# Kernel tuning notes

Hardware: AMD Instinct MI355X
Metric: run time of the kernel (lower is better)

The kernel has to match this reference:

```python
import jax, jax.numpy as jnp
import numpy as np

N_NODES = 50000
N_EDGES = 500000
H = 128
N_LAYERS = 3


def _mlp_params(key, in_dim, h_dim, out_dim):
    k1, k2 = jax.random.split(key)
    s1 = 1.0 / np.sqrt(in_dim)
    s2 = 1.0 / np.sqrt(h_dim)
    return (jax.random.uniform(k1, (in_dim, h_dim), jnp.float32, -s1, s1),
            jnp.zeros((h_dim,), jnp.float32),
            jax.random.uniform(k2, (h_dim, out_dim), jnp.float32, -s2, s2),
            jnp.zeros((out_dim,), jnp.float32))


def setup_inputs() -> dict:
    key = jax.random.key(0)
    ks = jax.random.split(key, 8)
    x = jax.random.normal(ks[0], (N_NODES, H), jnp.float32)
    edge_attr = jax.random.normal(ks[1], (N_EDGES, H), jnp.float32)
    pos = jax.random.normal(ks[2], (N_NODES, 3), jnp.float32)
    src = jax.random.randint(ks[3], (N_EDGES,), 0, N_NODES)
    # avoid self-loops so rel_dist > 0 (original assumes no zero-length edges)
    off = jax.random.randint(ks[4], (N_EDGES,), 1, N_NODES)
    dst = (src + off) % N_NODES
    edge_index = jnp.stack([src, dst]).astype(jnp.int64)
    # per-layer MLP params, stacked over layers
    msg, acc, nod = [], [], []
    for i in range(N_LAYERS):
        kk = jax.random.fold_in(ks[5], i)
        ka, kb, kc = jax.random.split(kk, 3)
        msg.append(_mlp_params(ka, 3 * H, H, H))       # message_mlp
        acc.append(_mlp_params(kb, H, 2 * H, 1))       # accl_mlp
        nod.append(_mlp_params(kc, 2 * H, 2 * H, H))   # node_mlp
    stack = lambda ps: tuple(jnp.stack([p[j] for p in ps]) for j in range(4))
    mW1, mb1, mW2, mb2 = stack(msg)
    aW1, ab1, aW2, ab2 = stack(acc)
    nW1, nb1, nW2, nb2 = stack(nod)
    return dict(x=x, edge_index=edge_index, edge_attr=edge_attr, pos=pos,
                msg_W1=mW1, msg_b1=mb1, msg_W2=mW2, msg_b2=mb2,
                acc_W1=aW1, acc_b1=ab1, acc_W2=aW2, acc_b2=ab2,
                node_W1=nW1, node_b1=nb1, node_W2=nW2, node_b2=nb2)


def _mlp(h, W1, b1, W2, b2):
    return jax.nn.relu(h @ W1 + b1) @ W2 + b2


def reference(x, edge_index, edge_attr, pos,
              msg_W1, msg_b1, msg_W2, msg_b2,
              acc_W1, acc_b1, acc_W2, acc_b2,
              node_W1, node_b1, node_W2, node_b2):
    src, dst = edge_index[0], edge_index[1]
    n = x.shape[0]
    deg = jax.ops.segment_sum(jnp.ones((src.shape[0],), x.dtype), dst, num_segments=n)
    denom = jnp.maximum(deg, 1.0)[:, None]
    for l in range(N_LAYERS):
        # message: cat(x_i=dst, x_j=src, edge_attr) -> MLP
        m_in = jnp.concatenate([x[dst], x[src], edge_attr], axis=-1)  # [E, 3H]
        m = _mlp(m_in, msg_W1[l], msg_b1[l], msg_W2[l], msg_b2[l])    # [E, H]
        # equivariant acceleration update
        w = _mlp(m, acc_W1[l], acc_b1[l], acc_W2[l], acc_b2[l])       # [E, 1]
        rel = pos[src] - pos[dst]                                     # [E, 3]
        dist = jnp.sqrt(jnp.sum(rel * rel, axis=-1, keepdims=True))
        acc_e = w * rel / dist
        pos = pos + jax.ops.segment_sum(acc_e, dst, num_segments=n) / denom
        # node update (beta_x = 1.0 -> x_out = x_update)
        intra = jax.ops.segment_sum(m, dst, num_segments=n) / denom   # [N, H]
        x = _mlp(jnp.concatenate([x, intra], axis=-1),
                 node_W1[l], node_b1[l], node_W2[l], node_b2[l])
    return pos
```

## Files before the change

### kernel.cpp

```cpp
#include <hip/hip_runtime.h>
#include <hip/hip_bf16.h>
#include <math.h>

#define N_NODES 50000
#define N_EDGES 500000
#define H 128
#define NL 3
#define SCAN_B 256
#define NCHUNK ((N_NODES + SCAN_B - 1) / SCAN_B)

typedef short short8v __attribute__((ext_vector_type(8)));
typedef float f32x4 __attribute__((ext_vector_type(4)));
typedef unsigned short ushort8v __attribute__((ext_vector_type(8)));
typedef unsigned short ushort4v __attribute__((ext_vector_type(4)));

__device__ __forceinline__ unsigned short f2b(float f) {
  __hip_bfloat16 h = __float2bfloat16(f);
  return __builtin_bit_cast(unsigned short, h);
}
__device__ __forceinline__ float b2f(unsigned short s) {
  unsigned u = (unsigned)s << 16;
  return __builtin_bit_cast(float, u);
}


__global__ void k_deg_i(const int* __restrict__ dst, int* __restrict__ degC) {
  int e = blockIdx.x * blockDim.x + threadIdx.x;
  if (e < N_EDGES) atomicAdd(&degC[dst[e]], 1);
}

__global__ void k_inv(const int* __restrict__ degC, float* __restrict__ invd) {
  int i = blockIdx.x * blockDim.x + threadIdx.x;
  if (i < N_NODES) invd[i] = 1.0f / fmaxf((float)degC[i], 1.0f);
}

__global__ void k_scan1(const int* __restrict__ degC, int* __restrict__ cursor,
                        int* __restrict__ chunkSum) {
  __shared__ int s[SCAN_B];
  int t = threadIdx.x, i = blockIdx.x * SCAN_B + t;
  int v = (i < N_NODES) ? degC[i] : 0;
  s[t] = v;
  __syncthreads();
  for (int o = 1; o < SCAN_B; o <<= 1) {
    int u = (t >= o) ? s[t - o] : 0;
    __syncthreads();
    s[t] += u;
    __syncthreads();
  }
  if (i < N_NODES) cursor[i] = s[t] - v;
  if (t == SCAN_B - 1) chunkSum[blockIdx.x] = s[t];
}

__global__ void k_scan2(int* __restrict__ chunkSum) {
  __shared__ int s[SCAN_B];
  int t = threadIdx.x;
  int v = (t < NCHUNK) ? chunkSum[t] : 0;
  s[t] = v;
  __syncthreads();
  for (int o = 1; o < SCAN_B; o <<= 1) {
    int u = (t >= o) ? s[t - o] : 0;
    __syncthreads();
    s[t] += u;
    __syncthreads();
  }
  if (t < NCHUNK) chunkSum[t] = s[t] - v;
}

__global__ void k_scan3(int* __restrict__ cursor, const int* __restrict__ chunkSum) {
  int i = blockIdx.x * SCAN_B + threadIdx.x;
  if (i < N_NODES) cursor[i] += chunkSum[blockIdx.x];
}

__global__ void k_scatter_sort(const int* __restrict__ dst, int* __restrict__ cursor,
                               int* __restrict__ sorted) {
  int e = blockIdx.x * blockDim.x + threadIdx.x;
  if (e < N_EDGES) {
    int p = atomicAdd(&cursor[dst[e]], 1);
    sorted[p] = e;
  }
}


__global__ void k_cvt_x(const float* __restrict__ x, unsigned short* __restrict__ xb, int n4) {
  int i = blockIdx.x * blockDim.x + threadIdx.x;
  if (i < n4) {
    float4 v = ((const float4*)x)[i];
    ushort4v o;
    o[0] = f2b(v.x); o[1] = f2b(v.y); o[2] = f2b(v.z); o[3] = f2b(v.w);
    ((ushort4v*)xb)[i] = o;
  }
}

__global__ void k_cvt_wt(const float* __restrict__ src, unsigned short* __restrict__ dst,
                         int K, int N, int total) {
  int i = blockIdx.x * blockDim.x + threadIdx.x;
  if (i < total) {
    int l = i / (K * N);
    int rem = i - l * K * N;
    int k = rem / N;
    int n = rem - k * N;
    dst[((size_t)l * N + n) * K + k] = f2b(src[i]);
  }
}

#define MFMA_STEP(AP, APITCH, AKOFF, ACCN)                                         \
  { _Pragma("unroll")                                                              \
    for (int ks = 0; ks < 2; ++ks) {                                               \
      short8v af_ = *(const short8v*)&AP[(wv * 16 + ln15) * APITCH + (AKOFF) + ks * 32 + quad * 8]; \
      _Pragma("unroll")                                                            \
      for (int nt = 0; nt < 8; ++nt) {                                             \
        short8v bf_ = *(const short8v*)&sB[(nt * 16 + ln15) * 72 + ks * 32 + quad * 8]; \
        ACCN[nt] = __builtin_amdgcn_mfma_f32_16x16x32_bf16(af_, bf_, ACCN[nt], 0, 0, 0); \
      } } }

#define STAGE_B(EXPR)                                                              \
  { _Pragma("unroll")                                                              \
    for (int i_ = 0; i_ < 4; ++i_) {                                               \
      int flat_ = tid + i_ * 256;                                                  \
      int n = flat_ >> 3, seg = flat_ & 7;                                         \
      *(float4*)&sB[n * 72 + seg * 8] = *(const float4*)&(EXPR);                   \
    } }


__launch_bounds__(256, 4)
__global__ void k_xab(const unsigned short* __restrict__ xb,
                      const unsigned short* __restrict__ mW1t,
                      unsigned short* __restrict__ xab)
{
  __shared__ unsigned short sB[128 * 72];
  const int tid = threadIdx.x;
  const int n0 = blockIdx.x * 64;
  const int wv = tid >> 6, lane = tid & 63, quad = lane >> 4, ln15 = lane & 15;
  const int arow = min(n0 + wv * 16 + ln15, N_NODES - 1);

  short8v afr[2][2];
#pragma unroll
  for (int c = 0; c < 2; ++c)
#pragma unroll
    for (int ks = 0; ks < 2; ++ks)
      afr[c][ks] = *(const short8v*)&xb[(size_t)arow * H + c * 64 + ks * 32 + quad * 8];

  for (int h = 0; h < 2; ++h) {
    f32x4 acc[8];
#pragma unroll
    for (int nt = 0; nt < 8; ++nt) acc[nt] = (f32x4){0.f, 0.f, 0.f, 0.f};
    for (int c = 0; c < 2; ++c) {
      STAGE_B(mW1t[(size_t)n * 384 + h * 128 + c * 64 + seg * 8])
      __syncthreads();
#pragma unroll
      for (int ks = 0; ks < 2; ++ks) {
#pragma unroll
        for (int nt = 0; nt < 8; ++nt) {
          short8v bf = *(const short8v*)&sB[(nt * 16 + ln15) * 72 + ks * 32 + quad * 8];
          acc[nt] = __builtin_amdgcn_mfma_f32_16x16x32_bf16(afr[c][ks], bf, acc[nt], 0, 0, 0);
        }
      }
      __syncthreads();
    }
#pragma unroll
    for (int nt = 0; nt < 8; ++nt) {
      int col = nt * 16 + ln15;
#pragma unroll
      for (int r = 0; r < 4; ++r) {
        int row = n0 + wv * 16 + quad * 4 + r;
        if (row < N_NODES)
          xab[(size_t)row * 256 + h * 128 + col] = f2b(acc[nt][r]);
      }
    }
  }
}


__launch_bounds__(256, 4)
__global__ void k_edge(const unsigned short* __restrict__ xab,
                       const float* __restrict__ pos,
                       const float* __restrict__ eattr,
                       const int* __restrict__ srcI,
                       const int* __restrict__ dstI,
                       const int* __restrict__ sorted,
                       const unsigned short* __restrict__ mW1t, const float* __restrict__ mb1,
                       const unsigned short* __restrict__ mW2t, const float* __restrict__ mb2,
                       const unsigned short* __restrict__ aW1t, const float* __restrict__ ab1,
                       const float* __restrict__ aW2, const float* __restrict__ ab2,
                       float* __restrict__ intra,
                       float* __restrict__ pdelta,
                       int do_intra)
{
  __shared__ unsigned short sB[128 * 72];
  __shared__ unsigned short sM[64 * 136];
  __shared__ int sEid[64], sSrc[64], sDst[64];
  __shared__ float sW[64];
  __shared__ float sPE[64 * 3];

  const int tid = threadIdx.x;
  const int e0 = blockIdx.x * 64;
  const int nv = min(N_EDGES - e0, 64);
  if (tid < 64) {
    int idx = min(e0 + tid, N_EDGES - 1);
    int eid = sorted[idx];
    sEid[tid] = eid; sSrc[tid] = srcI[eid]; sDst[tid] = dstI[eid];
  }
  __syncthreads();

  const int wv = tid >> 6, lane = tid & 63, quad = lane >> 4, ln15 = lane & 15;

#pragma unroll
  for (int i_ = 0; i_ < 4; ++i_) {
    int flat = tid + i_ * 256;
    int row = flat >> 4, sg = flat & 15;
    ushort8v a = *(const ushort8v*)&xab[(size_t)sDst[row] * 256 + sg * 8];
    ushort8v b = *(const ushort8v*)&xab[(size_t)sSrc[row] * 256 + 128 + sg * 8];
    ushort8v o;
#pragma unroll
    for (int j = 0; j < 8; ++j) o[j] = f2b(b2f(a[j]) + b2f(b[j]));
    *(ushort8v*)&sM[row * 136 + sg * 8] = o;
  }

  f32x4 acc[8];
#pragma unroll
  for (int nt = 0; nt < 8; ++nt) acc[nt] = (f32x4){0.f, 0.f, 0.f, 0.f};

  const float* aep = eattr + (size_t)sEid[wv * 16 + ln15] * H;
  for (int c = 0; c < 2; ++c) {
    float4 q0 = *(const float4*)(aep + c * 64 + quad * 8);
    float4 q1 = *(const float4*)(aep + c * 64 + quad * 8 + 4);
    float4 q2 = *(const float4*)(aep + c * 64 + 32 + quad * 8);
    float4 q3 = *(const float4*)(aep + c * 64 + 32 + quad * 8 + 4);
    STAGE_B(mW1t[(size_t)n * 384 + 256 + c * 64 + seg * 8])
    __syncthreads();
    short8v af0, af1;
    af0[0] = (short)f2b(q0.x); af0[1] = (short)f2b(q0.y);
    af0[2] = (short)f2b(q0.z); af0[3] = (short)f2b(q0.w);
    af0[4] = (short)f2b(q1.x); af0[5] = (short)f2b(q1.y);
    af0[6] = (short)f2b(q1.z); af0[7] = (short)f2b(q1.w);
    af1[0] = (short)f2b(q2.x); af1[1] = (short)f2b(q2.y);
    af1[2] = (short)f2b(q2.z); af1[3] = (short)f2b(q2.w);
    af1[4] = (short)f2b(q3.x); af1[5] = (short)f2b(q3.y);
    af1[6] = (short)f2b(q3.z); af1[7] = (short)f2b(q3.w);
#pragma unroll
    for (int nt = 0; nt < 8; ++nt) {
      short8v bf = *(const short8v*)&sB[(nt * 16 + ln15) * 72 + quad * 8];
      acc[nt] = __builtin_amdgcn_mfma_f32_16x16x32_bf16(af0, bf, acc[nt], 0, 0, 0);
    }
#pragma unroll
    for (int nt = 0; nt < 8; ++nt) {
      short8v bf = *(const short8v*)&sB[(nt * 16 + ln15) * 72 + 32 + quad * 8];
      acc[nt] = __builtin_amdgcn_mfma_f32_16x16x32_bf16(af1, bf, acc[nt], 0, 0, 0);
    }
    __syncthreads();
  }

#pragma unroll
  for (int nt = 0; nt < 8; ++nt) {
    int col = nt * 16 + ln15;
    float bb = mb1[col];
#pragma unroll
    for (int r = 0; r < 4; ++r) {
      int row = wv * 16 + quad * 4 + r;
      float xv = b2f(sM[row * 136 + col]);
      sM[row * 136 + col] = f2b(fmaxf(acc[nt][r] + xv + bb, 0.f));
      acc[nt][r] = 0.f;
    }
  }
  __syncthreads();

  for (int c = 0; c < 2; ++c) {
    STAGE_B(mW2t[(size_t)n * 128 + c * 64 + seg * 8])
    __syncthreads();
    MFMA_STEP(sM, 136, c * 64, acc)
    __syncthreads();
  }

#pragma unroll
  for (int nt = 0; nt < 8; ++nt) {
    int col = nt * 16 + ln15;
    float bb = mb2[col];
#pragma unroll
    for (int r = 0; r < 4; ++r) {
      int row = wv * 16 + quad * 4 + r;
      sM[row * 136 + col] = f2b(acc[nt][r] + bb);
    }
  }
  __syncthreads();

  float wp0 = 0.f, wp1 = 0.f, wp2 = 0.f, wp3 = 0.f;
  for (int h = 0; h < 2; ++h) {
#pragma unroll
    for (int nt = 0; nt < 8; ++nt) acc[nt] = (f32x4){0.f, 0.f, 0.f, 0.f};
    for (int c = 0; c < 2; ++c) {
      STAGE_B(aW1t[((size_t)h * 128 + n) * 128 + c * 64 + seg * 8])
      __syncthreads();
      MFMA_STEP(sM, 136, c * 64, acc)
      __syncthreads();
    }
#pragma unroll
    for (int nt = 0; nt < 8; ++nt) {
      int col = h * 128 + nt * 16 + ln15;
      float bb = ab1[col], a2 = aW2[col];
      wp0 += fmaxf(acc[nt][0] + bb, 0.f) * a2;
      wp1 += fmaxf(acc[nt][1] + bb, 0.f) * a2;
      wp2 += fmaxf(acc[nt][2] + bb, 0.f) * a2;
      wp3 += fmaxf(acc[nt][3] + bb, 0.f) * a2;
    }
  }
#pragma unroll
  for (int m = 1; m <= 8; m <<= 1) {
    wp0 += __shfl_xor(wp0, m, 64);
    wp1 += __shfl_xor(wp1, m, 64);
    wp2 += __shfl_xor(wp2, m, 64);
    wp3 += __shfl_xor(wp3, m, 64);
  }
  if (ln15 == 0) {
    float b2 = ab2[0];
    sW[wv * 16 + quad * 4 + 0] = wp0 + b2;
    sW[wv * 16 + quad * 4 + 1] = wp1 + b2;
    sW[wv * 16 + quad * 4 + 2] = wp2 + b2;
    sW[wv * 16 + quad * 4 + 3] = wp3 + b2;
  }
  __syncthreads();

  if (tid < nv) {
    int s = sSrc[tid], d = sDst[tid];
    float rx = pos[s * 3 + 0] - pos[d * 3 + 0];
    float ry = pos[s * 3 + 1] - pos[d * 3 + 1];
    float rz = pos[s * 3 + 2] - pos[d * 3 + 2];
    float dist = sqrtf(rx * rx + ry * ry + rz * rz);
    float cf = sW[tid] / dist;
    sPE[tid * 3 + 0] = cf * rx;
    sPE[tid * 3 + 1] = cf * ry;
    sPE[tid * 3 + 2] = cf * rz;
  }
  __syncthreads();

  if (tid < 3) {
    float run = 0.0f;
    int cur = -2;
    for (int e = 0; e < 64; ++e) {
      int d = (e < nv) ? sDst[e] : -1;
      if (d != cur) {
        if (cur >= 0 && run != 0.0f) atomicAdd(&pdelta[cur * 3 + tid], run);
        run = 0.0f;
        cur = d;
      }
      if (d >= 0) run += sPE[e * 3 + tid];
    }
    if (cur >= 0 && run != 0.0f) atomicAdd(&pdelta[cur * 3 + tid], run);
  }

  if (do_intra) {
    int f = tid & 127;
    int hf = tid >> 7;
    int eBeg = hf * 32, eEnd = eBeg + 32;
    float run = 0.0f;
    int cur = -2;
    for (int e = eBeg; e < eEnd; ++e) {
      int d = (e < nv) ? sDst[e] : -1;
      if (d != cur) {
        if (cur >= 0 && run != 0.0f) atomicAdd(&intra[(size_t)cur * H + f], run);
        run = 0.0f;
        cur = d;
      }
      if (d >= 0) run += b2f(sM[e * 136 + f]);
    }
    if (cur >= 0 && run != 0.0f) atomicAdd(&intra[(size_t)cur * H + f], run);
  }
}


__launch_bounds__(256, 3)
__global__ void k_node(const unsigned short* __restrict__ xb,
                       const float* __restrict__ intra,
                       const float* __restrict__ invd,
                       const unsigned short* __restrict__ nW1t, const float* __restrict__ nb1,
                       const unsigned short* __restrict__ nW2t, const float* __restrict__ nb2,
                       const float* __restrict__ pos_in,
                       const float* __restrict__ pdelta,
                       unsigned short* __restrict__ xb_out,
                       float* __restrict__ pos_out,
                       int compute_x)
{
  __shared__ unsigned short sA[64 * 72];
  __shared__ unsigned short sB[128 * 72];
  __shared__ unsigned short sH[64 * 136];
  const int tid = threadIdx.x;
  const int n0 = blockIdx.x * 64;

  if (tid < 192) {
    int n = n0 + tid / 3, cc = tid % 3;
    if (n < N_NODES)
      pos_out[n * 3 + cc] = pos_in[n * 3 + cc] + pdelta[n * 3 + cc] * invd[n];
  }
  if (!compute_x) return;

  const int wv = tid >> 6, lane = tid & 63, quad = lane >> 4, ln15 = lane & 15;

  f32x4 xacc[8];
#pragma unroll
  for (int nt = 0; nt < 8; ++nt) xacc[nt] = (f32x4){0.f, 0.f, 0.f, 0.f};

  f32x4 acc[8];
  for (int h = 0; h < 2; ++h) {
#pragma unroll
    for (int nt = 0; nt < 8; ++nt) acc[nt] = (f32x4){0.f, 0.f, 0.f, 0.f};
    for (int c = 0; c < 4; ++c) {
#pragma unroll
      for (int i_ = 0; i_ < 2; ++i_) {
        int flat_ = tid + i_ * 256;
        int row = flat_ >> 3, seg = flat_ & 7;
        int n = min(n0 + row, N_NODES - 1);
        if (c < 2) {
          *(float4*)&sA[row * 72 + seg * 8] =
              *(const float4*)&xb[(size_t)n * H + c * 64 + seg * 8];
        } else {
          const float* ip = intra + (size_t)n * H + (c - 2) * 64 + seg * 8;
          float iv = invd[n];
          float4 p0 = *(const float4*)ip;
          float4 p1 = *(const float4*)(ip + 4);
          ushort8v v;
          v[0] = f2b(p0.x * iv); v[1] = f2b(p0.y * iv);
          v[2] = f2b(p0.z * iv); v[3] = f2b(p0.w * iv);
          v[4] = f2b(p1.x * iv); v[5] = f2b(p1.y * iv);
          v[6] = f2b(p1.z * iv); v[7] = f2b(p1.w * iv);
          *(ushort8v*)&sA[row * 72 + seg * 8] = v;
        }
      }
      STAGE_B(nW1t[((size_t)h * 128 + n) * 256 + c * 64 + seg * 8])
      __syncthreads();
      MFMA_STEP(sA, 72, 0, acc)
      __syncthreads();
    }
#pragma unroll
    for (int nt = 0; nt < 8; ++nt) {
      int col = nt * 16 + ln15;
      float bb = nb1[h * 128 + col];
#pragma unroll
      for (int r = 0; r < 4; ++r) {
        int row = wv * 16 + quad * 4 + r;
        sH[row * 136 + col] = f2b(fmaxf(acc[nt][r] + bb, 0.f));
      }
    }
    __syncthreads();
    for (int c2 = 0; c2 < 2; ++c2) {
      STAGE_B(nW2t[(size_t)n * 256 + h * 128 + c2 * 64 + seg * 8])
      __syncthreads();
      MFMA_STEP(sH, 136, c2 * 64, xacc)
      __syncthreads();
    }
  }
#pragma unroll
  for (int nt = 0; nt < 8; ++nt) {
    int col = nt * 16 + ln15;
    float bb = nb2[col];
#pragma unroll
    for (int r = 0; r < 4; ++r) {
      int row = n0 + wv * 16 + quad * 4 + r;
      if (row < N_NODES)
        xb_out[(size_t)row * H + col] = f2b(xacc[nt][r] + bb);
    }
  }
}

extern "C" void kernel_launch(void* const* d_in, const int* in_sizes, int n_in,
                              void* d_out, int out_size, void* d_ws, size_t ws_size,
                              hipStream_t stream) {
  const float* x0    = (const float*)d_in[0];
  const int*   eidx  = (const int*)d_in[1];
  const float* eattr = (const float*)d_in[2];
  const float* pos0  = (const float*)d_in[3];
  const float* mW1 = (const float*)d_in[4];
  const float* mb1 = (const float*)d_in[5];
  const float* mW2 = (const float*)d_in[6];
  const float* mb2 = (const float*)d_in[7];
  const float* aW1 = (const float*)d_in[8];
  const float* ab1 = (const float*)d_in[9];
  const float* aW2 = (const float*)d_in[10];
  const float* ab2 = (const float*)d_in[11];
  const float* nW1 = (const float*)d_in[12];
  const float* nb1 = (const float*)d_in[13];
  const float* nW2 = (const float*)d_in[14];
  const float* nb2 = (const float*)d_in[15];
  const int* srcI = eidx;
  const int* dstI = eidx + N_EDGES;

  char* wsb = (char*)d_ws;
  int*   degC    = (int*)wsb;                     wsb += (size_t)N_NODES * 4;
  int*   cursor  = (int*)wsb;                     wsb += (size_t)N_NODES * 4;
  int*   chunkS  = (int*)wsb;                     wsb += 256 * 4;
  int*   sorted  = (int*)wsb;                     wsb += (size_t)N_EDGES * 4;
  float* invd    = (float*)wsb;                   wsb += (size_t)N_NODES * 4;
  float* pdelta  = (float*)wsb;                   wsb += (size_t)3 * N_NODES * 4;
  float* pos_a   = (float*)wsb;                   wsb += (size_t)3 * N_NODES * 4;
  float* pos_b   = (float*)wsb;                   wsb += (size_t)3 * N_NODES * 4;
  float* intra   = (float*)wsb;                   wsb += (size_t)N_NODES * H * 4;
  unsigned short* xb0  = (unsigned short*)wsb;    wsb += (size_t)N_NODES * H * 2;
  unsigned short* xb_a = (unsigned short*)wsb;    wsb += (size_t)N_NODES * H * 2;
  unsigned short* xb_b = (unsigned short*)wsb;    wsb += (size_t)N_NODES * H * 2;
  unsigned short* xabW = (unsigned short*)wsb;    wsb += (size_t)N_NODES * 256 * 2;
  unsigned short* mW1t = (unsigned short*)wsb;    wsb += (size_t)NL * 128 * 384 * 2;
  unsigned short* mW2t = (unsigned short*)wsb;    wsb += (size_t)NL * 128 * 128 * 2;
  unsigned short* aW1t = (unsigned short*)wsb;    wsb += (size_t)NL * 256 * 128 * 2;
  unsigned short* nW1t = (unsigned short*)wsb;    wsb += (size_t)NL * 256 * 256 * 2;
  unsigned short* nW2t = (unsigned short*)wsb;    wsb += (size_t)NL * 128 * 256 * 2;

  hipMemsetAsync(degC, 0, N_NODES * sizeof(int), stream);
  k_deg_i<<<(N_EDGES + 255) / 256, 256, 0, stream>>>(dstI, degC);
  k_inv<<<(N_NODES + 255) / 256, 256, 0, stream>>>(degC, invd);
  k_scan1<<<NCHUNK, SCAN_B, 0, stream>>>(degC, cursor, chunkS);
  k_scan2<<<1, SCAN_B, 0, stream>>>(chunkS);
  k_scan3<<<NCHUNK, SCAN_B, 0, stream>>>(cursor, chunkS);
  k_scatter_sort<<<(N_EDGES + 255) / 256, 256, 0, stream>>>(dstI, cursor, sorted);

  {
    int n4 = N_NODES * H / 4;
    k_cvt_x<<<(n4 + 255) / 256, 256, 0, stream>>>(x0, xb0, n4);
    int t1 = NL * 384 * 128;
    k_cvt_wt<<<(t1 + 255) / 256, 256, 0, stream>>>(mW1, mW1t, 384, 128, t1);
    int t2 = NL * 128 * 128;
    k_cvt_wt<<<(t2 + 255) / 256, 256, 0, stream>>>(mW2, mW2t, 128, 128, t2);
    int t3 = NL * 128 * 256;
    k_cvt_wt<<<(t3 + 255) / 256, 256, 0, stream>>>(aW1, aW1t, 128, 256, t3);
    int t4 = NL * 256 * 256;
    k_cvt_wt<<<(t4 + 255) / 256, 256, 0, stream>>>(nW1, nW1t, 256, 256, t4);
    int t5 = NL * 256 * 128;
    k_cvt_wt<<<(t5 + 255) / 256, 256, 0, stream>>>(nW2, nW2t, 256, 128, t5);
  }

  const unsigned short* xc = xb0;
  const float* pc = pos0;
  float* pos_out_final = (float*)d_out;

  for (int l = 0; l < NL; ++l) {
    int last = (l == NL - 1);
    hipMemsetAsync(pdelta, 0, 3 * N_NODES * sizeof(float), stream);
    if (!last)
      hipMemsetAsync(intra, 0, (size_t)N_NODES * H * sizeof(float), stream);

    k_xab<<<(N_NODES + 63) / 64, 256, 0, stream>>>(
        xc, mW1t + (size_t)l * 128 * 384, xabW);

    k_edge<<<(N_EDGES + 63) / 64, 256, 0, stream>>>(
        xabW, pc, eattr, srcI, dstI, sorted,
        mW1t + (size_t)l * 128 * 384, mb1 + (size_t)l * 128,
        mW2t + (size_t)l * 128 * 128, mb2 + (size_t)l * 128,
        aW1t + (size_t)l * 256 * 128, ab1 + (size_t)l * 256,
        aW2 + (size_t)l * 256, ab2 + l,
        intra, pdelta, last ? 0 : 1);

    float* pn = last ? pos_out_final : (l == 0 ? pos_a : pos_b);
    unsigned short* xn = (l == 0) ? xb_a : xb_b;
    k_node<<<(N_NODES + 63) / 64, 256, 0, stream>>>(
        xc, intra, invd,
        nW1t + (size_t)l * 256 * 256, nb1 + (size_t)l * 256,
        nW2t + (size_t)l * 128 * 256, nb2 + (size_t)l * 128,
        pc, pdelta, xn, pn, last ? 0 : 1);

    xc = xn;
    pc = pn;
  }
}
```

Before: 1.466 ms.

## Load MFMA weight fragments directly from global memory, drop LDS staging

Removes shared-memory staging of weight tiles (STAGE_B plus barriers) in k_xab, k_edge and k_node, so MFMA B-fragments are read straight from global/L2, and raises the launch-bounds occupancy targets. The k_edge grid gets an XCD-aware block remap so contiguous edge chunks run on the same XCD. The mb1 bias is folded into the precomputed xab projection, and k_node keeps its A fragments in registers. The goal is fewer barriers, less LDS traffic and higher occupancy, at the cost of repeated, less coalesced global weight loads that depend on cache hits, plus more register pressure.

Measured after the change: 2.543 ms. +73.5%, slower.

```diff
diff --git a/kernel.cpp b/kernel.cpp
--- a/kernel.cpp
+++ b/kernel.cpp
@@ -103,31 +103,23 @@
   }
 }
 
-#define MFMA_STEP(AP, APITCH, AKOFF, ACCN)                                         \
+#define MFMA_STEP_G(AP, APITCH, AKOFF, BP, BPITCH, BKOFF, ACCN)                    \
   { _Pragma("unroll")                                                              \
-    for (int ks = 0; ks < 2; ++ks) {                                               \
-      short8v af_ = *(const short8v*)&AP[(wv * 16 + ln15) * APITCH + (AKOFF) + ks * 32 + quad * 8]; \
+    for (int ks_ = 0; ks_ < 2; ++ks_) {                                            \
+      short8v af_ = *(const short8v*)&AP[(wv * 16 + ln15) * (APITCH) + (AKOFF) + ks_ * 32 + quad * 8]; \
       _Pragma("unroll")                                                            \
-      for (int nt = 0; nt < 8; ++nt) {                                             \
-        short8v bf_ = *(const short8v*)&sB[(nt * 16 + ln15) * 72 + ks * 32 + quad * 8]; \
-        ACCN[nt] = __builtin_amdgcn_mfma_f32_16x16x32_bf16(af_, bf_, ACCN[nt], 0, 0, 0); \
+      for (int nt_ = 0; nt_ < 8; ++nt_) {                                          \
+        short8v bf_ = *(const short8v*)&BP[(size_t)(nt_ * 16 + ln15) * (BPITCH) + (BKOFF) + ks_ * 32 + quad * 8]; \
+        ACCN[nt_] = __builtin_amdgcn_mfma_f32_16x16x32_bf16(af_, bf_, ACCN[nt_], 0, 0, 0); \
       } } }
 
-#define STAGE_B(EXPR)                                                              \
-  { _Pragma("unroll")                                                              \
-    for (int i_ = 0; i_ < 4; ++i_) {                                               \
-      int flat_ = tid + i_ * 256;                                                  \
-      int n = flat_ >> 3, seg = flat_ & 7;                                         \
-      *(float4*)&sB[n * 72 + seg * 8] = *(const float4*)&(EXPR);                   \
-    } }
-
-
-__launch_bounds__(256, 4)
+
+__launch_bounds__(256, 6)
 __global__ void k_xab(const unsigned short* __restrict__ xb,
                       const unsigned short* __restrict__ mW1t,
+                      const float* __restrict__ mb1,
                       unsigned short* __restrict__ xab)
 {
-  __shared__ unsigned short sB[128 * 72];
   const int tid = threadIdx.x;
   const int n0 = blockIdx.x * 64;
   const int wv = tid >> 6, lane = tid & 63, quad = lane >> 4, ln15 = lane & 15;
@@ -140,45 +132,43 @@
     for (int ks = 0; ks < 2; ++ks)
       afr[c][ks] = *(const short8v*)&xb[(size_t)arow * H + c * 64 + ks * 32 + quad * 8];
 
+#pragma unroll
   for (int h = 0; h < 2; ++h) {
     f32x4 acc[8];
 #pragma unroll
     for (int nt = 0; nt < 8; ++nt) acc[nt] = (f32x4){0.f, 0.f, 0.f, 0.f};
-    for (int c = 0; c < 2; ++c) {
-      STAGE_B(mW1t[(size_t)n * 384 + h * 128 + c * 64 + seg * 8])
-      __syncthreads();
-#pragma unroll
-      for (int ks = 0; ks < 2; ++ks) {
+#pragma unroll
+    for (int c = 0; c < 2; ++c)
+#pragma unroll
+      for (int ks = 0; ks < 2; ++ks)
 #pragma unroll
         for (int nt = 0; nt < 8; ++nt) {
-          short8v bf = *(const short8v*)&sB[(nt * 16 + ln15) * 72 + ks * 32 + quad * 8];
+          short8v bf = *(const short8v*)&mW1t[(size_t)(nt * 16 + ln15) * 384 + h * 128 + c * 64 + ks * 32 + quad * 8];
           acc[nt] = __builtin_amdgcn_mfma_f32_16x16x32_bf16(afr[c][ks], bf, acc[nt], 0, 0, 0);
         }
-      }
-      __syncthreads();
-    }
 #pragma unroll
     for (int nt = 0; nt < 8; ++nt) {
       int col = nt * 16 + ln15;
+      float bb = (h == 0) ? mb1[col] : 0.f;
 #pragma unroll
       for (int r = 0; r < 4; ++r) {
         int row = n0 + wv * 16 + quad * 4 + r;
         if (row < N_NODES)
-          xab[(size_t)row * 256 + h * 128 + col] = f2b(acc[nt][r]);
+          xab[(size_t)row * 256 + h * 128 + col] = f2b(acc[nt][r] + bb);
       }
     }
   }
 }
 
 
-__launch_bounds__(256, 4)
+__launch_bounds__(256, 6)
 __global__ void k_edge(const unsigned short* __restrict__ xab,
                        const float* __restrict__ pos,
                        const float* __restrict__ eattr,
                        const int* __restrict__ srcI,
                        const int* __restrict__ dstI,
                        const int* __restrict__ sorted,
-                       const unsigned short* __restrict__ mW1t, const float* __restrict__ mb1,
+                       const unsigned short* __restrict__ mW1t,
                        const unsigned short* __restrict__ mW2t, const float* __restrict__ mb2,
                        const unsigned short* __restrict__ aW1t, const float* __restrict__ ab1,
                        const float* __restrict__ aW2, const float* __restrict__ ab2,
@@ -186,14 +176,17 @@
                        float* __restrict__ pdelta,
                        int do_intra)
 {
-  __shared__ unsigned short sB[128 * 72];
   __shared__ unsigned short sM[64 * 136];
   __shared__ int sEid[64], sSrc[64], sDst[64];
   __shared__ float sW[64];
   __shared__ float sPE[64 * 3];
 
   const int tid = threadIdx.x;
-  const int e0 = blockIdx.x * 64;
+  const int nwg = gridDim.x;
+  const int q_ = nwg >> 3, r_ = nwg & 7;
+  const int xcd = blockIdx.x & 7, bidx = blockIdx.x >> 3;
+  const int bid = (xcd < r_ ? xcd * (q_ + 1) : r_ * (q_ + 1) + (xcd - r_) * q_) + bidx;
+  const int e0 = bid * 64;
   const int nv = min(N_EDGES - e0, 64);
   if (tid < 64) {
     int idx = min(e0 + tid, N_EDGES - 1);
@@ -221,13 +214,12 @@
   for (int nt = 0; nt < 8; ++nt) acc[nt] = (f32x4){0.f, 0.f, 0.f, 0.f};
 
   const float* aep = eattr + (size_t)sEid[wv * 16 + ln15] * H;
+#pragma unroll
   for (int c = 0; c < 2; ++c) {
     float4 q0 = *(const float4*)(aep + c * 64 + quad * 8);
     float4 q1 = *(const float4*)(aep + c * 64 + quad * 8 + 4);
     float4 q2 = *(const float4*)(aep + c * 64 + 32 + quad * 8);
     float4 q3 = *(const float4*)(aep + c * 64 + 32 + quad * 8 + 4);
-    STAGE_B(mW1t[(size_t)n * 384 + 256 + c * 64 + seg * 8])
-    __syncthreads();
     short8v af0, af1;
     af0[0] = (short)f2b(q0.x); af0[1] = (short)f2b(q0.y);
     af0[2] = (short)f2b(q0.z); af0[3] = (short)f2b(q0.w);
@@ -239,37 +231,35 @@
     af1[6] = (short)f2b(q3.z); af1[7] = (short)f2b(q3.w);
 #pragma unroll
     for (int nt = 0; nt < 8; ++nt) {
-      short8v bf = *(const short8v*)&sB[(nt * 16 + ln15) * 72 + quad * 8];
+      short8v bf = *(const short8v*)&mW1t[(size_t)(nt * 16 + ln15) * 384 + 256 + c * 64 + quad * 8];
       acc[nt] = __builtin_amdgcn_mfma_f32_16x16x32_bf16(af0, bf, acc[nt], 0, 0, 0);
     }
 #pragma unroll
     for (int nt = 0; nt < 8; ++nt) {
-      short8v bf = *(const short8v*)&sB[(nt * 16 + ln15) * 72 + 32 + quad * 8];
+      short8v bf = *(const short8v*)&mW1t[(size_t)(nt * 16 + ln15) * 384 + 256 + c * 64 + 32 + quad * 8];
       acc[nt] = __builtin_amdgcn_mfma_f32_16x16x32_bf16(af1, bf, acc[nt], 0, 0, 0);
     }
-    __syncthreads();
-  }
+  }
+  __syncthreads();
 
 #pragma unroll
   for (int nt = 0; nt < 8; ++nt) {
     int col = nt * 16 + ln15;
-    float bb = mb1[col];
 #pragma unroll
     for (int r = 0; r < 4; ++r) {
       int row = wv * 16 + quad * 4 + r;
       float xv = b2f(sM[row * 136 + col]);
-      sM[row * 136 + col] = f2b(fmaxf(acc[nt][r] + xv + bb, 0.f));
+      sM[row * 136 + col] = f2b(fmaxf(acc[nt][r] + xv, 0.f));
       acc[nt][r] = 0.f;
     }
   }
   __syncthreads();
 
+#pragma unroll
   for (int c = 0; c < 2; ++c) {
-    STAGE_B(mW2t[(size_t)n * 128 + c * 64 + seg * 8])
-    __syncthreads();
-    MFMA_STEP(sM, 136, c * 64, acc)
-    __syncthreads();
-  }
+    MFMA_STEP_G(sM, 136, c * 64, mW2t, 128, c * 64, acc)
+  }
+  __syncthreads();
 
 #pragma unroll
   for (int nt = 0; nt < 8; ++nt) {
@@ -284,14 +274,13 @@
   __syncthreads();
 
   float wp0 = 0.f, wp1 = 0.f, wp2 = 0.f, wp3 = 0.f;
+#pragma unroll
   for (int h = 0; h < 2; ++h) {
 #pragma unroll
     for (int nt = 0; nt < 8; ++nt) acc[nt] = (f32x4){0.f, 0.f, 0.f, 0.f};
+#pragma unroll
     for (int c = 0; c < 2; ++c) {
-      STAGE_B(aW1t[((size_t)h * 128 + n) * 128 + c * 64 + seg * 8])
-      __syncthreads();
-      MFMA_STEP(sM, 136, c * 64, acc)
-      __syncthreads();
+      MFMA_STEP_G(sM, 136, c * 64, (aW1t + (size_t)h * 128 * 128), 128, c * 64, acc)
     }
 #pragma unroll
     for (int nt = 0; nt < 8; ++nt) {
@@ -367,7 +356,7 @@
 }
 
 
-__launch_bounds__(256, 3)
+__launch_bounds__(256, 4)
 __global__ void k_node(const unsigned short* __restrict__ xb,
                        const float* __restrict__ intra,
                        const float* __restrict__ invd,
@@ -379,8 +368,6 @@
                        float* __restrict__ pos_out,
                        int compute_x)
 {
-  __shared__ unsigned short sA[64 * 72];
-  __shared__ unsigned short sB[128 * 72];
   __shared__ unsigned short sH[64 * 136];
   const int tid = threadIdx.x;
   const int n0 = blockIdx.x * 64;
@@ -393,42 +380,53 @@
   if (!compute_x) return;
 
   const int wv = tid >> 6, lane = tid & 63, quad = lane >> 4, ln15 = lane & 15;
+  const int arow = min(n0 + wv * 16 + ln15, N_NODES - 1);
+
+  short8v xfr[2][2];
+#pragma unroll
+  for (int c = 0; c < 2; ++c)
+#pragma unroll
+    for (int ks = 0; ks < 2; ++ks)
+      xfr[c][ks] = *(const short8v*)&xb[(size_t)arow * H + c * 64 + ks * 32 + quad * 8];
+
+  const float iv = invd[arow];
+  short8v ifr[2][2];
+#pragma unroll
+  for (int c = 0; c < 2; ++c)
+#pragma unroll
+    for (int ks = 0; ks < 2; ++ks) {
+      const float* ip = intra + (size_t)arow * H + c * 64 + ks * 32 + quad * 8;
+      float4 p0 = *(const float4*)ip;
+      float4 p1 = *(const float4*)(ip + 4);
+      short8v v;
+      v[0] = (short)f2b(p0.x * iv); v[1] = (short)f2b(p0.y * iv);
+      v[2] = (short)f2b(p0.z * iv); v[3] = (short)f2b(p0.w * iv);
+      v[4] = (short)f2b(p1.x * iv); v[5] = (short)f2b(p1.y * iv);
+      v[6] = (short)f2b(p1.z * iv); v[7] = (short)f2b(p1.w * iv);
+      ifr[c][ks] = v;
+    }
 
   f32x4 xacc[8];
 #pragma unroll
   for (int nt = 0; nt < 8; ++nt) xacc[nt] = (f32x4){0.f, 0.f, 0.f, 0.f};
 
-  f32x4 acc[8];
+#pragma unroll
   for (int h = 0; h < 2; ++h) {
+    f32x4 acc[8];
 #pragma unroll
     for (int nt = 0; nt < 8; ++nt) acc[nt] = (f32x4){0.f, 0.f, 0.f, 0.f};
-    for (int c = 0; c < 4; ++c) {
-#pragma unroll
-      for (int i_ = 0; i_ < 2; ++i_) {
-        int flat_ = tid + i_ * 256;
-        int row = flat_ >> 3, seg = flat_ & 7;
-        int n = min(n0 + row, N_NODES - 1);
-        if (c < 2) {
-          *(float4*)&sA[row * 72 + seg * 8] =
-              *(const float4*)&xb[(size_t)n * H + c * 64 + seg * 8];
-        } else {
-          const float* ip = intra + (size_t)n * H + (c - 2) * 64 + seg * 8;
-          float iv = invd[n];
-          float4 p0 = *(const float4*)ip;
-          float4 p1 = *(const float4*)(ip + 4);
-          ushort8v v;
-          v[0] = f2b(p0.x * iv); v[1] = f2b(p0.y * iv);
-          v[2] = f2b(p0.z * iv); v[3] = f2b(p0.w * iv);
-          v[4] = f2b(p1.x * iv); v[5] = f2b(p1.y * iv);
-          v[6] = f2b(p1.z * iv); v[7] = f2b(p1.w * iv);
-          *(ushort8v*)&sA[row * 72 + seg * 8] = v;
+#pragma unroll
+    for (int c = 0; c < 4; ++c)
+#pragma unroll
+      for (int ks = 0; ks < 2; ++ks) {
+        short8v af = (c < 2) ? xfr[c][ks] : ifr[c - 2][ks];
+#pragma unroll
+        for (int nt = 0; nt < 8; ++nt) {
+          short8v bf = *(const short8v*)&nW1t[(size_t)(h * 128 + nt * 16 + ln15) * 256 + c * 64 + ks * 32 + quad * 8];
+          acc[nt] = __builtin_amdgcn_mfma_f32_16x16x32_bf16(af, bf, acc[nt], 0, 0, 0);
         }
       }
-      STAGE_B(nW1t[((size_t)h * 128 + n) * 256 + c * 64 + seg * 8])
-      __syncthreads();
-      MFMA_STEP(sA, 72, 0, acc)
-      __syncthreads();
-    }
+    __syncthreads();
 #pragma unroll
     for (int nt = 0; nt < 8; ++nt) {
       int col = nt * 16 + ln15;
@@ -440,11 +438,9 @@
       }
     }
     __syncthreads();
+#pragma unroll
     for (int c2 = 0; c2 < 2; ++c2) {
-      STAGE_B(nW2t[(size_t)n * 256 + h * 128 + c2 * 64 + seg * 8])
-      __syncthreads();
-      MFMA_STEP(sH, 136, c2 * 64, xacc)
-      __syncthreads();
+      MFMA_STEP_G(sH, 136, c2 * 64, nW2t, 256, h * 128 + c2 * 64, xacc)
     }
   }
 #pragma unroll
@@ -536,11 +532,11 @@
       hipMemsetAsync(intra, 0, (size_t)N_NODES * H * sizeof(float), stream);
 
     k_xab<<<(N_NODES + 63) / 64, 256, 0, stream>>>(
-        xc, mW1t + (size_t)l * 128 * 384, xabW);
+        xc, mW1t + (size_t)l * 128 * 384, mb1 + (size_t)l * 128, xabW);
 
     k_edge<<<(N_EDGES + 63) / 64, 256, 0, stream>>>(
         xabW, pc, eattr, srcI, dstI, sorted,
-        mW1t + (size_t)l * 128 * 384, mb1 + (size_t)l * 128,
+        mW1t + (size_t)l * 128 * 384,
         mW2t + (size_t)l * 128 * 128, mb2 + (size_t)l * 128,
         aW1t + (size_t)l * 256 * 128, ab1 + (size_t)l * 256,
         aW2 + (size_t)l * 256, ab2 + l,
```

## Presort edge data and replace atomic scatter with deterministic CSR segment reduction

Applied to the files above, without the earlier changes.

Adds a one-time permutation kernel that gathers edge attributes (converted to bf16) and src/dst indices into dst-sorted order, so the edge kernel reads them contiguously. The edge kernel now stages full 128-wide weight tiles in shared memory, folds the message bias into the precomputed node projection, and writes per-edge messages and scalar weights to global buffers instead of doing atomic adds. A new segment kernel walks the CSR ranges to reduce messages and position deltas per node without atomics or memsets. This trades atomic contention for an extra round trip of edge-sized buffers through memory and serial per-node loops with one thread per feature.

After: 1.606 ms. 9.6% more time.

```diff
diff --git a/kernel.cpp b/kernel.cpp
--- a/kernel.cpp
+++ b/kernel.cpp
@@ -77,6 +77,26 @@
   if (e < N_EDGES) {
     int p = atomicAdd(&cursor[dst[e]], 1);
     sorted[p] = e;
+  }
+}
+
+
+__global__ void k_perm(const float* __restrict__ eattr, const int* __restrict__ sorted,
+                       const int* __restrict__ srcI, const int* __restrict__ dstI,
+                       unsigned short* __restrict__ eattrS,
+                       int* __restrict__ srcS, int* __restrict__ dstS) {
+  int g = blockIdx.x * 16 + (threadIdx.x >> 4);
+  int seg = threadIdx.x & 15;
+  if (g < N_EDGES) {
+    int eid = sorted[g];
+    const float* ep = eattr + (size_t)eid * H + seg * 8;
+    float4 p0 = *(const float4*)ep;
+    float4 p1 = *(const float4*)(ep + 4);
+    ushort8v v;
+    v[0] = f2b(p0.x); v[1] = f2b(p0.y); v[2] = f2b(p0.z); v[3] = f2b(p0.w);
+    v[4] = f2b(p1.x); v[5] = f2b(p1.y); v[6] = f2b(p1.z); v[7] = f2b(p1.w);
+    *(ushort8v*)&eattrS[(size_t)g * H + seg * 8] = v;
+    if (seg == 0) { srcS[g] = srcI[eid]; dstS[g] = dstI[eid]; }
   }
 }
 
@@ -103,6 +123,7 @@
   }
 }
 
+
 #define MFMA_STEP(AP, APITCH, AKOFF, ACCN)                                         \
   { _Pragma("unroll")                                                              \
     for (int ks = 0; ks < 2; ++ks) {                                               \
@@ -121,10 +142,32 @@
       *(float4*)&sB[n * 72 + seg * 8] = *(const float4*)&(EXPR);                   \
     } }
 
+#define STAGE128(BASE, PITCH, KOFF)                                                \
+  { _Pragma("unroll")                                                              \
+    for (int i_ = 0; i_ < 8; ++i_) {                                               \
+      int flat_ = tid + i_ * 256;                                                  \
+      int n_ = flat_ >> 4, sg_ = flat_ & 15;                                       \
+      *(float4*)&sB[n_ * 136 + sg_ * 8] =                                          \
+          *(const float4*)&(BASE)[(size_t)n_ * (PITCH) + (KOFF) + sg_ * 8];        \
+    } }
+
+#define MFMA_FULL(AP, ACCN)                                                        \
+  { _Pragma("unroll")                                                              \
+    for (int c_ = 0; c_ < 2; ++c_)                                                 \
+      _Pragma("unroll")                                                            \
+      for (int ks_ = 0; ks_ < 2; ++ks_) {                                          \
+        short8v af_ = *(const short8v*)&AP[(wv * 16 + ln15) * 136 + c_ * 64 + ks_ * 32 + quad * 8]; \
+        _Pragma("unroll")                                                          \
+        for (int nt_ = 0; nt_ < 8; ++nt_) {                                        \
+          short8v bf_ = *(const short8v*)&sB[(nt_ * 16 + ln15) * 136 + c_ * 64 + ks_ * 32 + quad * 8]; \
+          ACCN[nt_] = __builtin_amdgcn_mfma_f32_16x16x32_bf16(af_, bf_, ACCN[nt_], 0, 0, 0); \
+        } } }
+
 
 __launch_bounds__(256, 4)
 __global__ void k_xab(const unsigned short* __restrict__ xb,
                       const unsigned short* __restrict__ mW1t,
+                      const float* __restrict__ mb1,
                       unsigned short* __restrict__ xab)
 {
   __shared__ unsigned short sB[128 * 72];
@@ -160,49 +203,60 @@
 #pragma unroll
     for (int nt = 0; nt < 8; ++nt) {
       int col = nt * 16 + ln15;
+      float bb = (h == 0) ? mb1[col] : 0.f;
 #pragma unroll
       for (int r = 0; r < 4; ++r) {
         int row = n0 + wv * 16 + quad * 4 + r;
         if (row < N_NODES)
-          xab[(size_t)row * 256 + h * 128 + col] = f2b(acc[nt][r]);
+          xab[(size_t)row * 256 + h * 128 + col] = f2b(acc[nt][r] + bb);
       }
     }
   }
 }
 
 
-__launch_bounds__(256, 4)
-__global__ void k_edge(const unsigned short* __restrict__ xab,
-                       const float* __restrict__ pos,
-                       const float* __restrict__ eattr,
-                       const int* __restrict__ srcI,
-                       const int* __restrict__ dstI,
-                       const int* __restrict__ sorted,
-                       const unsigned short* __restrict__ mW1t, const float* __restrict__ mb1,
-                       const unsigned short* __restrict__ mW2t, const float* __restrict__ mb2,
-                       const unsigned short* __restrict__ aW1t, const float* __restrict__ ab1,
-                       const float* __restrict__ aW2, const float* __restrict__ ab2,
-                       float* __restrict__ intra,
-                       float* __restrict__ pdelta,
-                       int do_intra)
+__launch_bounds__(256, 3)
+__global__ void k_edge_m(const unsigned short* __restrict__ xab,
+                         const unsigned short* __restrict__ eattrS,
+                         const int* __restrict__ srcS,
+                         const int* __restrict__ dstS,
+                         const unsigned short* __restrict__ mW1t,
+                         const unsigned short* __restrict__ mW2t,
+                         const float* __restrict__ mb2,
+                         const unsigned short* __restrict__ aW1t,
+                         const float* __restrict__ ab1,
+                         const float* __restrict__ aW2, const float* __restrict__ ab2,
+                         unsigned short* __restrict__ mS,
+                         float* __restrict__ wS,
+                         int do_m)
 {
-  __shared__ unsigned short sB[128 * 72];
   __shared__ unsigned short sM[64 * 136];
-  __shared__ int sEid[64], sSrc[64], sDst[64];
+  __shared__ unsigned short sB[128 * 136];
+  __shared__ int sSrc[64], sDst[64];
   __shared__ float sW[64];
-  __shared__ float sPE[64 * 3];
 
   const int tid = threadIdx.x;
-  const int e0 = blockIdx.x * 64;
-  const int nv = min(N_EDGES - e0, 64);
+  const int nwg = gridDim.x;
+  const int q_ = nwg >> 3, r_ = nwg & 7;
+  const int xcd = blockIdx.x & 7, bidx = blockIdx.x >> 3;
+  const int bid = (xcd < r_ ? xcd * (q_ + 1) : r_ * (q_ + 1) + (xcd - r_) * q_) + bidx;
+  const int e0 = bid * 64;
+
   if (tid < 64) {
     int idx = min(e0 + tid, N_EDGES - 1);
-    int eid = sorted[idx];
-    sEid[tid] = eid; sSrc[tid] = srcI[eid]; sDst[tid] = dstI[eid];
+    sSrc[tid] = srcS[idx]; sDst[tid] = dstS[idx];
   }
   __syncthreads();
 
   const int wv = tid >> 6, lane = tid & 63, quad = lane >> 4, ln15 = lane & 15;
+
+  const int slotA = min(e0 + wv * 16 + ln15, N_EDGES - 1);
+  short8v afr[2][2];
+#pragma unroll
+  for (int c = 0; c < 2; ++c)
+#pragma unroll
+    for (int ks = 0; ks < 2; ++ks)
+      afr[c][ks] = *(const short8v*)&eattrS[(size_t)slotA * H + c * 64 + ks * 32 + quad * 8];
 
 #pragma unroll
   for (int i_ = 0; i_ < 4; ++i_) {
@@ -216,60 +270,42 @@
     *(ushort8v*)&sM[row * 136 + sg * 8] = o;
   }
 
+  STAGE128(mW1t, 384, 256)
+  __syncthreads();
+
   f32x4 acc[8];
 #pragma unroll
   for (int nt = 0; nt < 8; ++nt) acc[nt] = (f32x4){0.f, 0.f, 0.f, 0.f};
 
-  const float* aep = eattr + (size_t)sEid[wv * 16 + ln15] * H;
-  for (int c = 0; c < 2; ++c) {
-    float4 q0 = *(const float4*)(aep + c * 64 + quad * 8);
-    float4 q1 = *(const float4*)(aep + c * 64 + quad * 8 + 4);
-    float4 q2 = *(const float4*)(aep + c * 64 + 32 + quad * 8);
-    float4 q3 = *(const float4*)(aep + c * 64 + 32 + quad * 8 + 4);
-    STAGE_B(mW1t[(size_t)n * 384 + 256 + c * 64 + seg * 8])
-    __syncthreads();
-    short8v af0, af1;
-    af0[0] = (short)f2b(q0.x); af0[1] = (short)f2b(q0.y);
-    af0[2] = (short)f2b(q0.z); af0[3] = (short)f2b(q0.w);
-    af0[4] = (short)f2b(q1.x); af0[5] = (short)f2b(q1.y);
-    af0[6] = (short)f2b(q1.z); af0[7] = (short)f2b(q1.w);
-    af1[0] = (short)f2b(q2.x); af1[1] = (short)f2b(q2.y);
-    af1[2] = (short)f2b(q2.z); af1[3] = (short)f2b(q2.w);
-    af1[4] = (short)f2b(q3.x); af1[5] = (short)f2b(q3.y);
-    af1[6] = (short)f2b(q3.z); af1[7] = (short)f2b(q3.w);
-#pragma unroll
-    for (int nt = 0; nt < 8; ++nt) {
-      short8v bf = *(const short8v*)&sB[(nt * 16 + ln15) * 72 + quad * 8];
-      acc[nt] = __builtin_amdgcn_mfma_f32_16x16x32_bf16(af0, bf, acc[nt], 0, 0, 0);
-    }
-#pragma unroll
-    for (int nt = 0; nt < 8; ++nt) {
-      short8v bf = *(const short8v*)&sB[(nt * 16 + ln15) * 72 + 32 + quad * 8];
-      acc[nt] = __builtin_amdgcn_mfma_f32_16x16x32_bf16(af1, bf, acc[nt], 0, 0, 0);
-    }
-    __syncthreads();
-  }
+#pragma unroll
+  for (int c = 0; c < 2; ++c)
+#pragma unroll
+    for (int ks = 0; ks < 2; ++ks) {
+#pragma unroll
+      for (int nt = 0; nt < 8; ++nt) {
+        short8v bf = *(const short8v*)&sB[(nt * 16 + ln15) * 136 + c * 64 + ks * 32 + quad * 8];
+        acc[nt] = __builtin_amdgcn_mfma_f32_16x16x32_bf16(afr[c][ks], bf, acc[nt], 0, 0, 0);
+      }
+    }
 
 #pragma unroll
   for (int nt = 0; nt < 8; ++nt) {
     int col = nt * 16 + ln15;
-    float bb = mb1[col];
 #pragma unroll
     for (int r = 0; r < 4; ++r) {
       int row = wv * 16 + quad * 4 + r;
       float xv = b2f(sM[row * 136 + col]);
-      sM[row * 136 + col] = f2b(fmaxf(acc[nt][r] + xv + bb, 0.f));
+      sM[row * 136 + col] = f2b(fmaxf(acc[nt][r] + xv, 0.f));
       acc[nt][r] = 0.f;
     }
   }
   __syncthreads();
 
-  for (int c = 0; c < 2; ++c) {
-    STAGE_B(mW2t[(size_t)n * 128 + c * 64 + seg * 8])
-    __syncthreads();
-    MFMA_STEP(sM, 136, c * 64, acc)
-    __syncthreads();
-  }
+  STAGE128(mW2t, 128, 0)
+  __syncthreads();
+
+  MFMA_FULL(sM, acc)
+  __syncthreads();
 
 #pragma unroll
   for (int nt = 0; nt < 8; ++nt) {
@@ -281,21 +317,34 @@
       sM[row * 136 + col] = f2b(acc[nt][r] + bb);
     }
   }
+  STAGE128(aW1t, 128, 0)
   __syncthreads();
 
   float wp0 = 0.f, wp1 = 0.f, wp2 = 0.f, wp3 = 0.f;
-  for (int h = 0; h < 2; ++h) {
+  {
 #pragma unroll
     for (int nt = 0; nt < 8; ++nt) acc[nt] = (f32x4){0.f, 0.f, 0.f, 0.f};
-    for (int c = 0; c < 2; ++c) {
-      STAGE_B(aW1t[((size_t)h * 128 + n) * 128 + c * 64 + seg * 8])
-      __syncthreads();
-      MFMA_STEP(sM, 136, c * 64, acc)
-      __syncthreads();
-    }
+    MFMA_FULL(sM, acc)
 #pragma unroll
     for (int nt = 0; nt < 8; ++nt) {
-      int col = h * 128 + nt * 16 + ln15;
+      int col = nt * 16 + ln15;
+      float bb = ab1[col], a2 = aW2[col];
+      wp0 += fmaxf(acc[nt][0] + bb, 0.f) * a2;
+      wp1 += fmaxf(acc[nt][1] + bb, 0.f) * a2;
+      wp2 += fmaxf(acc[nt][2] + bb, 0.f) * a2;
+      wp3 += fmaxf(acc[nt][3] + bb, 0.f) * a2;
+    }
+  }
+  __syncthreads();
+  STAGE128((aW1t + (size_t)128 * 128), 128, 0)
+  __syncthreads();
+  {
+#pragma unroll
+    for (int nt = 0; nt < 8; ++nt) acc[nt] = (f32x4){0.f, 0.f, 0.f, 0.f};
+    MFMA_FULL(sM, acc)
+#pragma unroll
+    for (int nt = 0; nt < 8; ++nt) {
+      int col = 128 + nt * 16 + ln15;
       float bb = ab1[col], a2 = aW2[col];
       wp0 += fmaxf(acc[nt][0] + bb, 0.f) * a2;
       wp1 += fmaxf(acc[nt][1] + bb, 0.f) * a2;
@@ -317,52 +366,69 @@
     sW[wv * 16 + quad * 4 + 2] = wp2 + b2;
     sW[wv * 16 + quad * 4 + 3] = wp3 + b2;
   }
-  __syncthreads();
-
-  if (tid < nv) {
-    int s = sSrc[tid], d = sDst[tid];
-    float rx = pos[s * 3 + 0] - pos[d * 3 + 0];
-    float ry = pos[s * 3 + 1] - pos[d * 3 + 1];
-    float rz = pos[s * 3 + 2] - pos[d * 3 + 2];
-    float dist = sqrtf(rx * rx + ry * ry + rz * rz);
-    float cf = sW[tid] / dist;
-    sPE[tid * 3 + 0] = cf * rx;
-    sPE[tid * 3 + 1] = cf * ry;
-    sPE[tid * 3 + 2] = cf * rz;
-  }
-  __syncthreads();
-
-  if (tid < 3) {
-    float run = 0.0f;
-    int cur = -2;
-    for (int e = 0; e < 64; ++e) {
-      int d = (e < nv) ? sDst[e] : -1;
-      if (d != cur) {
-        if (cur >= 0 && run != 0.0f) atomicAdd(&pdelta[cur * 3 + tid], run);
-        run = 0.0f;
-        cur = d;
+
+  if (do_m) {
+#pragma unroll
+    for (int i_ = 0; i_ < 4; ++i_) {
+      int flat = tid + i_ * 256;
+      int row = flat >> 4, sg = flat & 15;
+      int slot = e0 + row;
+      if (slot < N_EDGES)
+        *(ushort8v*)&mS[(size_t)slot * H + sg * 8] =
+            *(const ushort8v*)&sM[row * 136 + sg * 8];
+    }
+  }
+  __syncthreads();
+  if (tid < 64 && e0 + tid < N_EDGES) wS[e0 + tid] = sW[tid];
+}
+
+
+__launch_bounds__(256, 8)
+__global__ void k_seg(const unsigned short* __restrict__ mS,
+                      const float* __restrict__ wS,
+                      const int* __restrict__ srcS,
+                      const float* __restrict__ pos,
+                      const int* __restrict__ cursor,
+                      float* __restrict__ intra,
+                      float* __restrict__ pdelta,
+                      int do_intra)
+{
+  const int n0 = blockIdx.x * 64;
+  const int tid = threadIdx.x;
+
+  if (tid < 128) {
+    if (!do_intra) return;
+    const int f = tid;
+    for (int j = 0; j < 64; ++j) {
+      int n = n0 + j;
+      if (n >= N_NODES) break;
+      int rs = (n == 0) ? 0 : cursor[n - 1];
+      int re = cursor[n];
+      float a = 0.f;
+      for (int s = rs; s < re; ++s) a += b2f(mS[(size_t)s * H + f]);
+      intra[(size_t)n * H + f] = a;
+    }
+  } else {
+    for (int idx = tid - 128; idx < 192; idx += 128) {
+      int n = n0 + idx / 3, c = idx % 3;
+      if (n >= N_NODES) continue;
+      int rs = (n == 0) ? 0 : cursor[n - 1];
+      int re = cursor[n];
+      float pd = pos[n * 3 + c];
+      float px = pos[n * 3 + 0], py = pos[n * 3 + 1], pz = pos[n * 3 + 2];
+      float a = 0.f;
+      for (int s = rs; s < re; ++s) {
+        int sn = srcS[s];
+        float rx = pos[sn * 3 + 0] - px;
+        float ry = pos[sn * 3 + 1] - py;
+        float rz = pos[sn * 3 + 2] - pz;
+        float dist = sqrtf(rx * rx + ry * ry + rz * rz);
+        float rc = (c == 0) ? rx : ((c == 1) ? ry : rz);
+        a += wS[s] * rc / dist;
       }
-      if (d >= 0) run += sPE[e * 3 + tid];
-    }
-    if (cur >= 0 && run != 0.0f) atomicAdd(&pdelta[cur * 3 + tid], run);
-  }
-
-  if (do_intra) {
-    int f = tid & 127;
-    int hf = tid >> 7;
-    int eBeg = hf * 32, eEnd = eBeg + 32;
-    float run = 0.0f;
-    int cur = -2;
-    for (int e = eBeg; e < eEnd; ++e) {
-      int d = (e < nv) ? sDst[e] : -1;
-      if (d != cur) {
-        if (cur >= 0 && run != 0.0f) atomicAdd(&intra[(size_t)cur * H + f], run);
-        run = 0.0f;
-        cur = d;
-      }
-      if (d >= 0) run += b2f(sM[e * 136 + f]);
-    }
-    if (cur >= 0 && run != 0.0f) atomicAdd(&intra[(size_t)cur * H + f], run);
+      (void)pd;
+      pdelta[n * 3 + c] = a;
+    }
   }
 }
 
@@ -496,6 +562,11 @@
   unsigned short* xb_a = (unsigned short*)wsb;    wsb += (size_t)N_NODES * H * 2;
   unsigned short* xb_b = (unsigned short*)wsb;    wsb += (size_t)N_NODES * H * 2;
   unsigned short* xabW = (unsigned short*)wsb;    wsb += (size_t)N_NODES * 256 * 2;
+  unsigned short* eattrS = (unsigned short*)wsb;  wsb += (size_t)N_EDGES * H * 2;
+  unsigned short* mS   = (unsigned short*)wsb;    wsb += (size_t)N_EDGES * H * 2;
+  int*   srcS    = (int*)wsb;                     wsb += (size_t)N_EDGES * 4;
+  int*   dstS    = (int*)wsb;                     wsb += (size_t)N_EDGES * 4;
+  float* wS      = (float*)wsb;                   wsb += (size_t)N_EDGES * 4;
   unsigned short* mW1t = (unsigned short*)wsb;    wsb += (size_t)NL * 128 * 384 * 2;
   unsigned short* mW2t = (unsigned short*)wsb;    wsb += (size_t)NL * 128 * 128 * 2;
   unsigned short* aW1t = (unsigned short*)wsb;    wsb += (size_t)NL * 256 * 128 * 2;
@@ -509,6 +580,9 @@
   k_scan2<<<1, SCAN_B, 0, stream>>>(chunkS);
   k_scan3<<<NCHUNK, SCAN_B, 0, stream>>>(cursor, chunkS);
   k_scatter_sort<<<(N_EDGES + 255) / 256, 256, 0, stream>>>(dstI, cursor, sorted);
+
+  k_perm<<<(N_EDGES * 16 + 255) / 256, 256, 0, stream>>>(
+      eattr, sorted, srcI, dstI, eattrS, srcS, dstS);
 
   {
     int n4 = N_NODES * H / 4;
@@ -531,20 +605,20 @@
 
   for (int l = 0; l < NL; ++l) {
     int last = (l == NL - 1);
-    hipMemsetAsync(pdelta, 0, 3 * N_NODES * sizeof(float), stream);
-    if (!last)
-      hipMemsetAsync(intra, 0, (size_t)N_NODES * H * sizeof(float), stream);
 
     k_xab<<<(N_NODES + 63) / 64, 256, 0, stream>>>(
-        xc, mW1t + (size_t)l * 128 * 384, xabW);
-
-    k_edge<<<(N_EDGES + 63) / 64, 256, 0, stream>>>(
-        xabW, pc, eattr, srcI, dstI, sorted,
-        mW1t + (size_t)l * 128 * 384, mb1 + (size_t)l * 128,
+        xc, mW1t + (size_t)l * 128 * 384, mb1 + (size_t)l * 128, xabW);
+
+    k_edge_m<<<(N_EDGES + 63) / 64, 256, 0, stream>>>(
+        xabW, eattrS, srcS, dstS,
+        mW1t + (size_t)l * 128 * 384,
         mW2t + (size_t)l * 128 * 128, mb2 + (size_t)l * 128,
         aW1t + (size_t)l * 256 * 128, ab1 + (size_t)l * 256,
         aW2 + (size_t)l * 256, ab2 + l,
-        intra, pdelta, last ? 0 : 1);
+        mS, wS, last ? 0 : 1);
+
+    k_seg<<<(N_NODES + 63) / 64, 256, 0, stream>>>(
+        mS, wS, srcS, pc, cursor, intra, pdelta, last ? 0 : 1);
 
     float* pn = last ? pos_out_final : (l == 0 ? pos_a : pos_b);
     unsigned short* xn = (l == 0) ? xb_a : xb_b;
```
